# Performance work log

Hardware: AMD Instinct MI355X
Metric: run time of the kernel (lower is better)

The kernel has to match this reference:

```python
import jax, jax.numpy as jnp
import numpy as np

NB_HEAD = 16
SIZE_PER_HEAD = 64


def setup_inputs() -> dict:
    key = jax.random.key(0)
    k1, k2 = jax.random.split(key)
    x = jax.random.normal(k1, (2, 2048, 1024), dtype=jnp.float32)
    kernel = jax.random.normal(k2, (3, 1024, NB_HEAD * SIZE_PER_HEAD), dtype=jnp.float32) * 0.02
    return {"x": x, "kernel": kernel}


def reference(x, kernel):
    B, S, D = x.shape
    H, dh = NB_HEAD, SIZE_PER_HEAD
    # QKV projections: [B,S,D] @ [D, H*dh] -> [B,S,H,dh] -> [B,H,S,dh]
    def proj(w):
        return jnp.einsum('bsd,de->bse', x, w).reshape(B, S, H, dh).transpose(0, 2, 1, 3)
    Q = proj(kernel[0])
    Ks = proj(kernel[1])
    V = proj(kernel[2])
    scores = jnp.einsum('bhqd,bhkd->bhqk', Q, Ks) / jnp.sqrt(jnp.float32(dh))
    attn = jax.nn.softmax(scores, axis=-1)
    z = jnp.einsum('bhqk,bhkd->bhqd', attn, V)  # [B,H,S,dh]
    return z.transpose(0, 2, 1, 3).reshape(B, S, H * dh)
```

## Files before the change

kernel.cpp:

```cpp
#include <hip/hip_runtime.h>
#include <hip/hip_bf16.h>

#define HB 16
#define DH 64
#define SQ 2048
#define BB 2

using f32x4 = __attribute__((ext_vector_type(4))) float;
using f32x16 = __attribute__((ext_vector_type(16))) float;
using s16x8 = __attribute__((ext_vector_type(8))) short;

__device__ __forceinline__ unsigned bfr(float f) {
    union { float f; unsigned u; } v; v.f = f;
    return (v.u + 0x7fffu + ((v.u >> 16) & 1u)) >> 16;
}
__device__ __forceinline__ unsigned pk2(float a, float b) { return bfr(a) | (bfr(b) << 16); }
__device__ __forceinline__ short f2bf(float f) { return (short)bfr(f); }

__device__ __forceinline__ int swz64(int r, int c) {
    return r * 64 + ((((c >> 3) ^ (r & 7)) & 7) << 3) + (c & 7);
}
__device__ __forceinline__ int swz32(int r, int c) {
    return r * 32 + ((((c >> 3) ^ ((r >> 1) & 3)) & 3) << 3) + (c & 7);
}

__device__ __forceinline__ void gll16(const short* g, short* l) {
    __builtin_amdgcn_global_load_lds(
        (const __attribute__((address_space(1))) unsigned int*)(uintptr_t)g,
        (__attribute__((address_space(3))) unsigned int*)(uintptr_t)l, 16, 0, 0);
}

__global__ __launch_bounds__(256) void cvt_x(const float* __restrict__ x, short* __restrict__ xb) {
    int i = (blockIdx.x * 256 + threadIdx.x) * 8;
    float4 v0 = *(const float4*)&x[i];
    float4 v1 = *(const float4*)&x[i + 4];
    uint4 u;
    u.x = pk2(v0.x, v0.y); u.y = pk2(v0.z, v0.w);
    u.z = pk2(v1.x, v1.y); u.w = pk2(v1.z, v1.w);
    *(uint4*)&xb[i] = u;
}

__device__ __forceinline__ int swzT(int n, int k) {
    return n * 64 + ((((k >> 3) ^ ((n >> 2) & 7)) & 7) << 3) + (k & 7);
}
__global__ __launch_bounds__(256) void cvt_wt(const float* __restrict__ w, short* __restrict__ wt) {
    __shared__ short T[64 * 64];
    int bid = blockIdx.x;
    int nt = bid & 15, kt = (bid >> 4) & 15, p = bid >> 8;
    const float* wp = w + p * 1048576 + (kt * 64) * 1024 + nt * 64;
    short* wtp = wt + p * 1048576 + (nt * 64) * 1024 + kt * 64;
    int t = threadIdx.x;
#pragma unroll
    for (int ps = 0; ps < 4; ps++) {
        int idx = ps * 1024 + t * 4;
        int r = idx >> 6, c = idx & 63;
        float4 v = *(const float4*)&wp[r * 1024 + c];
        T[swzT(c + 0, r)] = f2bf(v.x);
        T[swzT(c + 1, r)] = f2bf(v.y);
        T[swzT(c + 2, r)] = f2bf(v.z);
        T[swzT(c + 3, r)] = f2bf(v.w);
    }
    __syncthreads();
#pragma unroll
    for (int ps = 0; ps < 2; ps++) {
        int idx = ps * 2048 + t * 8;
        int n = idx >> 6, kc = idx & 63;
        s16x8 vv = *(const s16x8*)&T[swzT(n, kc)];
        *(s16x8*)&wtp[n * 1024 + kc] = vv;
    }
}

__global__ __launch_bounds__(512, 2) void qkv_gemm(
    const short* __restrict__ xb, const short* __restrict__ wt, short* __restrict__ ws)
{
    __shared__ short Xs[2][128 * 32];
    __shared__ short Ns[2][384 * 32];
    const int tid = threadIdx.x;
    const int wv = tid >> 6, ln = tid & 63;
    const int bid = blockIdx.x;
    const int swz = (bid & 7) * 32 + (bid >> 3);
    const int m0 = (swz & 31) * 128;
    const int n0 = (swz >> 5) * 128;

    const int wm = (wv >> 2) * 64, wn = (wv & 3) * 96;
    const int lr = ln & 15, lk = (ln >> 4) * 8;
    const int srow = tid >> 2;
    const int csw = (((tid & 3) ^ ((tid >> 3) & 3)) & 3) * 8;

    f32x4 acc[4][6] = {};

#define GSTAGE(k0_, bf_) do {                                                   \
        gll16(&xb[(m0 + srow) * 1024 + (k0_) + csw], &Xs[bf_][wv * 512]);       \
        _Pragma("unroll")                                                       \
        for (int p_ = 0; p_ < 3; p_++)                                          \
            gll16(&wt[p_ * 1048576 + (n0 + srow) * 1024 + (k0_) + csw],         \
                  &Ns[bf_][p_ * 4096 + wv * 512]);                              \
    } while (0)

#define GCOMP(bf_) do {                                                         \
        s16x8 af[4], bg[6];                                                     \
        _Pragma("unroll")                                                       \
        for (int i = 0; i < 4; i++)                                             \
            af[i] = *(const s16x8*)&Xs[bf_][swz32(wm + i * 16 + lr, lk)];       \
        _Pragma("unroll")                                                       \
        for (int j = 0; j < 6; j++)                                             \
            bg[j] = *(const s16x8*)&Ns[bf_][swz32(wn + j * 16 + lr, lk)];       \
        __builtin_amdgcn_s_setprio(1);                                          \
        _Pragma("unroll")                                                       \
        for (int i = 0; i < 4; i++)                                             \
            _Pragma("unroll")                                                   \
            for (int j = 0; j < 6; j++)                                         \
                acc[i][j] = __builtin_amdgcn_mfma_f32_16x16x32_bf16(af[i], bg[j], acc[i][j], 0, 0, 0); \
        __builtin_amdgcn_s_setprio(0);                                          \
    } while (0)

    GSTAGE(0, 0);
    __syncthreads();
    for (int t = 0; t < 32; t++) {
        int cur = t & 1;
        if (t < 31) GSTAGE((t + 1) * 32, cur ^ 1);
        GCOMP(cur);
        __syncthreads();
    }

    short* qws = ws;
    short* kws = ws + BB * HB * SQ * DH;
    short* vtw = ws + 2 * BB * HB * SQ * DH;
#pragma unroll
    for (int i = 0; i < 4; i++) {
#pragma unroll
        for (int r = 0; r < 4; r++) {
            int row = m0 + wm + i * 16 + (ln >> 4) * 4 + r;
            int b = row >> 11, s = row & 2047;
#pragma unroll
            for (int j = 0; j < 6; j++) {
                int c = wn + j * 16 + (ln & 15);
                int p = c >> 7;
                int gcol = n0 + (c & 127);
                int h = gcol >> 6, dhi = gcol & 63;
                float v = acc[i][j][r];
                if (p == 0)      qws[((b * HB + h) * SQ + s) * DH + dhi] = f2bf(v * 0.1803368801f);
                else if (p == 1) kws[((b * HB + h) * SQ + s) * DH + dhi] = f2bf(v);
                else             vtw[((b * HB + h) * DH + dhi) * SQ + s] = f2bf(v);
            }
        }
    }
#undef GSTAGE
#undef GCOMP
}

__global__ __launch_bounds__(512, 4) void attn(
    const short* __restrict__ qws, const short* __restrict__ kws,
    const short* __restrict__ vtw, float* __restrict__ out)
{
    __shared__ __align__(16) short smem[32768];
    __shared__ float Lx[4][32];
    const int tid = threadIdx.x, wv = tid >> 6, ln = tid & 63;
    const int ws_ = wv & 3, g = wv >> 2;
    const int bid = blockIdx.x;
    const int swz = (bid & 7) * 64 + (bid >> 3);
    const int qt = swz & 15, bh = swz >> 4;
    const short* Q = qws + bh * SQ * DH;
    const short* K = kws + bh * SQ * DH;
    const short* VT = vtw + bh * DH * SQ;
    const int lq = ln & 31, lg = ln >> 5;
    const int q0w = qt * 128 + ws_ * 32;
    const int kvbase = g * 1024;

    const int csw = ((ln & 7) ^ ((ln >> 3) & 7)) * 8;
    const int klo = (ln >> 3) * DH + csw;
    const int vlo = (ln >> 3) * SQ + csw;

    s16x8 qf[4];
#pragma unroll
    for (int ks = 0; ks < 4; ks++)
        qf[ks] = *(const s16x8*)&Q[(q0w + lq) * DH + ks * 16 + lg * 8];

    f32x16 o0 = {}, o1 = {};
    float l = 0.f;

#define STAGE(t, bf_) do {                                          \
        short* Kd = smem + g * 16384 + (bf_) * 8192;                \
        short* Vd = Kd + 4096;                                      \
        const short* Kt = K + (kvbase + (t) * 64) * DH;             \
        const short* Vt = VT + kvbase + (t) * 64;                   \
        _Pragma("unroll")                                           \
        for (int jj = 0; jj < 2; jj++) {                            \
            int run = ws_ * 2 + jj;                                 \
            gll16(Kt + run * 8 * DH + klo, Kd + run * 512);         \
            gll16(Vt + run * 8 * SQ + vlo, Vd + run * 512);         \
        }                                                           \
    } while (0)

#define COMPUTE(bf_) do {                                                      \
        const short* Kr = smem + g * 16384 + (bf_) * 8192;                     \
        const short* Vr = Kr + 4096;                                           \
        f32x16 s0 = {}, s1 = {};                                               \
        __builtin_amdgcn_s_setprio(1);                                         \
        _Pragma("unroll")                                                      \
        for (int ks = 0; ks < 4; ks++) {                                       \
            s16x8 ka0 = *(const s16x8*)&Kr[swz64(lq, ks * 16 + lg * 8)];       \
            s16x8 ka1 = *(const s16x8*)&Kr[swz64(32 + lq, ks * 16 + lg * 8)];  \
            s0 = __builtin_amdgcn_mfma_f32_32x32x16_bf16(ka0, qf[ks], s0, 0, 0, 0); \
            s1 = __builtin_amdgcn_mfma_f32_32x32x16_bf16(ka1, qf[ks], s1, 0, 0, 0); \
        }                                                                      \
        __builtin_amdgcn_s_setprio(0);                                         \
        float p[32];                                                           \
        _Pragma("unroll")                                                      \
        for (int i = 0; i < 16; i++) p[i] = __builtin_amdgcn_exp2f(s0[i]);     \
        _Pragma("unroll")                                                      \
        for (int i = 0; i < 16; i++) p[16 + i] = __builtin_amdgcn_exp2f(s1[i]); \
        float a0 = 0.f, a1 = 0.f, a2 = 0.f, a3 = 0.f;                          \
        _Pragma("unroll")                                                      \
        for (int i = 0; i < 32; i += 4) {                                      \
            a0 += p[i]; a1 += p[i + 1]; a2 += p[i + 2]; a3 += p[i + 3];        \
        }                                                                      \
        l += (a0 + a1) + (a2 + a3);                                            \
        unsigned u[16];                                                        \
        _Pragma("unroll")                                                      \
        for (int qd = 0; qd < 8; qd++) {                                       \
            asm("v_cvt_pk_bf16_f32 %0, %1, %2" : "=v"(u[qd * 2]) : "v"(p[qd * 4 + 0]), "v"(p[qd * 4 + 1])); \
            asm("v_cvt_pk_bf16_f32 %0, %1, %2" : "=v"(u[qd * 2 + 1]) : "v"(p[qd * 4 + 2]), "v"(p[qd * 4 + 3])); \
        }                                                                      \
        _Pragma("unroll")                                                      \
        for (int a = 0; a < 2; a++)                                            \
            _Pragma("unroll")                                                  \
            for (int m2 = 0; m2 < 2; m2++)                                     \
                _Pragma("unroll")                                              \
                for (int j = 0; j < 2; j++)                                    \
                    asm("v_permlane32_swap_b32 %0, %1"                         \
                        : "+v"(u[(a * 4 + 2 * m2) * 2 + j]), "+v"(u[(a * 4 + 2 * m2 + 1) * 2 + j])); \
        __builtin_amdgcn_s_setprio(1);                                         \
        _Pragma("unroll")                                                      \
        for (int ks = 0; ks < 4; ks++) {                                       \
            int a = ks >> 1, m2 = ks & 1;                                      \
            union { unsigned w[4]; s16x8 v; } pa;                              \
            pa.w[0] = u[(a * 4 + 2 * m2) * 2];                                 \
            pa.w[1] = u[(a * 4 + 2 * m2) * 2 + 1];                             \
            pa.w[2] = u[(a * 4 + 2 * m2 + 1) * 2];                             \
            pa.w[3] = u[(a * 4 + 2 * m2 + 1) * 2 + 1];                         \
            s16x8 vb0 = *(const s16x8*)&Vr[swz64(lq, ks * 16 + lg * 8)];       \
            s16x8 vb1 = *(const s16x8*)&Vr[swz64(32 + lq, ks * 16 + lg * 8)];  \
            o0 = __builtin_amdgcn_mfma_f32_32x32x16_bf16(pa.v, vb0, o0, 0, 0, 0); \
            o1 = __builtin_amdgcn_mfma_f32_32x32x16_bf16(pa.v, vb1, o1, 0, 0, 0); \
        }                                                                      \
        __builtin_amdgcn_s_setprio(0);                                         \
    } while (0)

    STAGE(0, 0);
    __syncthreads();
    for (int t = 0; t < 16; t++) {
        int cur = t & 1;
        if (t < 15) STAGE(t + 1, cur ^ 1);
        COMPUTE(cur);
        __syncthreads();
    }

    float lt = l + __shfl_xor(l, 32);
    float* Lf = (float*)smem;
    if (g == 1) {
#pragma unroll
        for (int r = 0; r < 16; r++) {
            Lf[ws_ * 1024 + r * 64 + ln] = o0[r];
            Lf[8192 + ws_ * 1024 + r * 64 + ln] = o1[r];
        }
        if (lg == 0) Lx[ws_][lq] = lt;
    }
    __syncthreads();
    if (g == 0) {
        float inv = 1.0f / (lt + Lx[ws_][lq]);
        const int b = bh >> 4, h = bh & 15;
#pragma unroll
        for (int r = 0; r < 16; r++) {
            int qrow = (r & 3) + 8 * (r >> 2) + 4 * lg;
            float iv = __shfl(inv, qrow);
            float* op = out + ((long)(b * SQ + q0w + qrow)) * 1024 + h * 64 + lq;
            op[0]  = (o0[r] + Lf[ws_ * 1024 + r * 64 + ln]) * iv;
            op[32] = (o1[r] + Lf[8192 + ws_ * 1024 + r * 64 + ln]) * iv;
        }
    }
#undef STAGE
#undef COMPUTE
}

extern "C" void kernel_launch(void* const* d_in, const int* in_sizes, int n_in,
                              void* d_out, int out_size, void* d_ws, size_t ws_size,
                              hipStream_t stream) {
    const float* x = (const float*)d_in[0];
    const float* w = (const float*)d_in[1];
    short* ws = (short*)d_ws;
    short* xbf = (short*)d_out;
    short* wtb = (short*)d_out + 4194304;
    cvt_x<<<2048, 256, 0, stream>>>(x, xbf);
    cvt_wt<<<768, 256, 0, stream>>>(w, wtb);
    qkv_gemm<<<256, 512, 0, stream>>>(xbf, wtb, ws);
    attn<<<512, 512, 0, stream>>>(ws, ws + BB * HB * SQ * DH,
                                  ws + 2 * BB * HB * SQ * DH, (float*)d_out);
}
```

Baseline: 97.87 us.

## Software-pipeline attention QK^T ahead of softmax-PV with triple buffering; fuse conversion kernels

```diff
diff --git a/kernel.cpp b/kernel.cpp
--- a/kernel.cpp
+++ b/kernel.cpp
@@ -30,26 +30,30 @@
         (__attribute__((address_space(3))) unsigned int*)(uintptr_t)l, 16, 0, 0);
 }
 
-__global__ __launch_bounds__(256) void cvt_x(const float* __restrict__ x, short* __restrict__ xb) {
-    int i = (blockIdx.x * 256 + threadIdx.x) * 8;
-    float4 v0 = *(const float4*)&x[i];
-    float4 v1 = *(const float4*)&x[i + 4];
-    uint4 u;
-    u.x = pk2(v0.x, v0.y); u.y = pk2(v0.z, v0.w);
-    u.z = pk2(v1.x, v1.y); u.w = pk2(v1.z, v1.w);
-    *(uint4*)&xb[i] = u;
-}
-
 __device__ __forceinline__ int swzT(int n, int k) {
     return n * 64 + ((((k >> 3) ^ ((n >> 2) & 7)) & 7) << 3) + (k & 7);
 }
-__global__ __launch_bounds__(256) void cvt_wt(const float* __restrict__ w, short* __restrict__ wt) {
+__global__ __launch_bounds__(256) void cvt_all(
+    const float* __restrict__ x, const float* __restrict__ w,
+    short* __restrict__ xb, short* __restrict__ wt)
+{
     __shared__ short T[64 * 64];
     int bid = blockIdx.x;
+    int t = threadIdx.x;
+    if (bid < 2048) {
+        int i = (bid * 256 + t) * 8;
+        float4 v0 = *(const float4*)&x[i];
+        float4 v1 = *(const float4*)&x[i + 4];
+        uint4 u;
+        u.x = pk2(v0.x, v0.y); u.y = pk2(v0.z, v0.w);
+        u.z = pk2(v1.x, v1.y); u.w = pk2(v1.z, v1.w);
+        *(uint4*)&xb[i] = u;
+        return;
+    }
+    bid -= 2048;
     int nt = bid & 15, kt = (bid >> 4) & 15, p = bid >> 8;
     const float* wp = w + p * 1048576 + (kt * 64) * 1024 + nt * 64;
     short* wtp = wt + p * 1048576 + (nt * 64) * 1024 + kt * 64;
-    int t = threadIdx.x;
 #pragma unroll
     for (int ps = 0; ps < 4; ps++) {
         int idx = ps * 1024 + t * 4;
@@ -149,11 +153,11 @@
 #undef GCOMP
 }
 
-__global__ __launch_bounds__(512, 4) void attn(
+__global__ __launch_bounds__(512) void attn(
     const short* __restrict__ qws, const short* __restrict__ kws,
     const short* __restrict__ vtw, float* __restrict__ out)
 {
-    __shared__ __align__(16) short smem[32768];
+    __shared__ __align__(16) short smem[24576];
     __shared__ float Lx[4][32];
     const int tid = threadIdx.x, wv = tid >> 6, ln = tid & 63;
     const int ws_ = wv & 3, g = wv >> 2;
@@ -167,9 +171,9 @@
     const int q0w = qt * 128 + ws_ * 32;
     const int kvbase = g * 1024;
 
-    const int csw = ((ln & 7) ^ ((ln >> 3) & 7)) * 8;
-    const int klo = (ln >> 3) * DH + csw;
-    const int vlo = (ln >> 3) * SQ + csw;
+    const int klo = (ws_ * 8 + (ln >> 3)) * DH + (((ln & 7) ^ ((ln >> 3) & 7)) & 7) * 8;
+    const int vr = ln >> 2;
+    const int vlo = (ws_ * 16 + vr) * SQ + (((ln & 3) ^ ((vr >> 1) & 3)) & 3) * 8;
 
     s16x8 qf[4];
 #pragma unroll
@@ -180,67 +184,57 @@
     float l = 0.f;
 
 #define STAGE(t, bf_) do {                                          \
-        short* Kd = smem + g * 16384 + (bf_) * 8192;                \
-        short* Vd = Kd + 4096;                                      \
-        const short* Kt = K + (kvbase + (t) * 64) * DH;             \
-        const short* Vt = VT + kvbase + (t) * 64;                   \
-        _Pragma("unroll")                                           \
-        for (int jj = 0; jj < 2; jj++) {                            \
-            int run = ws_ * 2 + jj;                                 \
-            gll16(Kt + run * 8 * DH + klo, Kd + run * 512);         \
-            gll16(Vt + run * 8 * SQ + vlo, Vd + run * 512);         \
-        }                                                           \
-    } while (0)
-
-#define COMPUTE(bf_) do {                                                      \
-        const short* Kr = smem + g * 16384 + (bf_) * 8192;                     \
-        const short* Vr = Kr + 4096;                                           \
-        f32x16 s0 = {}, s1 = {};                                               \
+        short* Kd = smem + g * 12288 + (bf_) * 4096;                \
+        const short* Kt = K + (kvbase + (t) * 32) * DH;             \
+        const short* Vt = VT + kvbase + (t) * 32;                   \
+        gll16(Kt + klo, Kd + ws_ * 512);                            \
+        gll16(Vt + vlo, Kd + 2048 + ws_ * 512);                     \
+    } while (0)
+
+#define QKT(bf_, S_) do {                                                      \
+        const short* Kr = smem + g * 12288 + (bf_) * 4096;                     \
         __builtin_amdgcn_s_setprio(1);                                         \
         _Pragma("unroll")                                                      \
         for (int ks = 0; ks < 4; ks++) {                                       \
-            s16x8 ka0 = *(const s16x8*)&Kr[swz64(lq, ks * 16 + lg * 8)];       \
-            s16x8 ka1 = *(const s16x8*)&Kr[swz64(32 + lq, ks * 16 + lg * 8)];  \
-            s0 = __builtin_amdgcn_mfma_f32_32x32x16_bf16(ka0, qf[ks], s0, 0, 0, 0); \
-            s1 = __builtin_amdgcn_mfma_f32_32x32x16_bf16(ka1, qf[ks], s1, 0, 0, 0); \
+            s16x8 ka = *(const s16x8*)&Kr[swz64(lq, ks * 16 + lg * 8)];        \
+            S_ = __builtin_amdgcn_mfma_f32_32x32x16_bf16(ka, qf[ks], S_, 0, 0, 0); \
         }                                                                      \
         __builtin_amdgcn_s_setprio(0);                                         \
-        float p[32];                                                           \
-        _Pragma("unroll")                                                      \
-        for (int i = 0; i < 16; i++) p[i] = __builtin_amdgcn_exp2f(s0[i]);     \
-        _Pragma("unroll")                                                      \
-        for (int i = 0; i < 16; i++) p[16 + i] = __builtin_amdgcn_exp2f(s1[i]); \
+    } while (0)
+
+#define SMPV(bf_, S_) do {                                                     \
+        const short* Vr = smem + g * 12288 + (bf_) * 4096 + 2048;              \
+        float p[16];                                                           \
+        _Pragma("unroll")                                                      \
+        for (int i = 0; i < 16; i++) p[i] = __builtin_amdgcn_exp2f(S_[i]);     \
         float a0 = 0.f, a1 = 0.f, a2 = 0.f, a3 = 0.f;                          \
         _Pragma("unroll")                                                      \
-        for (int i = 0; i < 32; i += 4) {                                      \
+        for (int i = 0; i < 16; i += 4) {                                      \
             a0 += p[i]; a1 += p[i + 1]; a2 += p[i + 2]; a3 += p[i + 3];        \
         }                                                                      \
         l += (a0 + a1) + (a2 + a3);                                            \
-        unsigned u[16];                                                        \
-        _Pragma("unroll")                                                      \
-        for (int qd = 0; qd < 8; qd++) {                                       \
+        unsigned u[8];                                                         \
+        _Pragma("unroll")                                                      \
+        for (int qd = 0; qd < 4; qd++) {                                       \
             asm("v_cvt_pk_bf16_f32 %0, %1, %2" : "=v"(u[qd * 2]) : "v"(p[qd * 4 + 0]), "v"(p[qd * 4 + 1])); \
             asm("v_cvt_pk_bf16_f32 %0, %1, %2" : "=v"(u[qd * 2 + 1]) : "v"(p[qd * 4 + 2]), "v"(p[qd * 4 + 3])); \
         }                                                                      \
         _Pragma("unroll")                                                      \
-        for (int a = 0; a < 2; a++)                                            \
+        for (int m2 = 0; m2 < 2; m2++)                                         \
             _Pragma("unroll")                                                  \
-            for (int m2 = 0; m2 < 2; m2++)                                     \
-                _Pragma("unroll")                                              \
-                for (int j = 0; j < 2; j++)                                    \
-                    asm("v_permlane32_swap_b32 %0, %1"                         \
-                        : "+v"(u[(a * 4 + 2 * m2) * 2 + j]), "+v"(u[(a * 4 + 2 * m2 + 1) * 2 + j])); \
+            for (int j = 0; j < 2; j++)                                        \
+                asm("v_permlane32_swap_b32 %0, %1"                             \
+                    : "+v"(u[(2 * m2) * 2 + j]), "+v"(u[(2 * m2 + 1) * 2 + j])); \
         __builtin_amdgcn_s_setprio(1);                                         \
         _Pragma("unroll")                                                      \
-        for (int ks = 0; ks < 4; ks++) {                                       \
-            int a = ks >> 1, m2 = ks & 1;                                      \
+        for (int ks = 0; ks < 2; ks++) {                                       \
             union { unsigned w[4]; s16x8 v; } pa;                              \
-            pa.w[0] = u[(a * 4 + 2 * m2) * 2];                                 \
-            pa.w[1] = u[(a * 4 + 2 * m2) * 2 + 1];                             \
-            pa.w[2] = u[(a * 4 + 2 * m2 + 1) * 2];                             \
-            pa.w[3] = u[(a * 4 + 2 * m2 + 1) * 2 + 1];                         \
-            s16x8 vb0 = *(const s16x8*)&Vr[swz64(lq, ks * 16 + lg * 8)];       \
-            s16x8 vb1 = *(const s16x8*)&Vr[swz64(32 + lq, ks * 16 + lg * 8)];  \
+            pa.w[0] = u[4 * ks + 0];                                           \
+            pa.w[1] = u[4 * ks + 1];                                           \
+            pa.w[2] = u[4 * ks + 2];                                           \
+            pa.w[3] = u[4 * ks + 3];                                           \
+            s16x8 vb0 = *(const s16x8*)&Vr[swz32(lq, ks * 16 + lg * 8)];       \
+            s16x8 vb1 = *(const s16x8*)&Vr[swz32(32 + lq, ks * 16 + lg * 8)];  \
             o0 = __builtin_amdgcn_mfma_f32_32x32x16_bf16(pa.v, vb0, o0, 0, 0, 0); \
             o1 = __builtin_amdgcn_mfma_f32_32x32x16_bf16(pa.v, vb1, o1, 0, 0, 0); \
         }                                                                      \
@@ -248,11 +242,21 @@
     } while (0)
 
     STAGE(0, 0);
+    STAGE(1, 1);
     __syncthreads();
-    for (int t = 0; t < 16; t++) {
-        int cur = t & 1;
-        if (t < 15) STAGE(t + 1, cur ^ 1);
-        COMPUTE(cur);
+    f32x16 sA = {}, sB = {};
+    QKT(0, sA);
+#pragma unroll
+    for (int t = 0; t < 32; t++) {
+        if (t < 30) STAGE(t + 2, (t + 2) % 3);
+        if (t < 31) {
+            if (t & 1) QKT((t + 1) % 3, sA);
+            else       QKT((t + 1) % 3, sB);
+        }
+        if (t & 1) SMPV(t % 3, sB);
+        else       SMPV(t % 3, sA);
+        if (t & 1) sB = (f32x16){};
+        else       sA = (f32x16){};
         __syncthreads();
     }
 
@@ -262,7 +266,7 @@
 #pragma unroll
         for (int r = 0; r < 16; r++) {
             Lf[ws_ * 1024 + r * 64 + ln] = o0[r];
-            Lf[8192 + ws_ * 1024 + r * 64 + ln] = o1[r];
+            Lf[4096 + ws_ * 1024 + r * 64 + ln] = o1[r];
         }
         if (lg == 0) Lx[ws_][lq] = lt;
     }
@@ -276,11 +280,12 @@
             float iv = __shfl(inv, qrow);
             float* op = out + ((long)(b * SQ + q0w + qrow)) * 1024 + h * 64 + lq;
             op[0]  = (o0[r] + Lf[ws_ * 1024 + r * 64 + ln]) * iv;
-            op[32] = (o1[r] + Lf[8192 + ws_ * 1024 + r * 64 + ln]) * iv;
+            op[32] = (o1[r] + Lf[4096 + ws_ * 1024 + r * 64 + ln]) * iv;
         }
     }
 #undef STAGE
-#undef COMPUTE
+#undef QKT
+#undef SMPV
 }
 
 extern "C" void kernel_launch(void* const* d_in, const int* in_sizes, int n_in,
@@ -291,8 +296,7 @@
     short* ws = (short*)d_ws;
     short* xbf = (short*)d_out;
     short* wtb = (short*)d_out + 4194304;
-    cvt_x<<<2048, 256, 0, stream>>>(x, xbf);
-    cvt_wt<<<768, 256, 0, stream>>>(w, wtb);
+    cvt_all<<<2816, 256, 0, stream>>>(x, w, xbf, wtb);
     qkv_gemm<<<256, 512, 0, stream>>>(xbf, wtb, ws);
     attn<<<512, 512, 0, stream>>>(ws, ws + BB * HB * SQ * DH,
                                   ws + 2 * BB * HB * SQ * DH, (float*)d_out);
```

New measurement: 94.59 us. 1.03x faster.
